# Performance work log

Hardware: AMD Instinct MI355X
Metric: run time of the kernel (lower is better)

Reference implementation:

```python
import jax, jax.numpy as jnp
import numpy as np

LEVELS = 6
_S = float(1.0 / np.sqrt(2.0))  # forward transform scales kernels by 1/sqrt(2)
# Complex Daubechies 6-tap filters (real, imag), pre-scaled for the forward DWT.
LO_R = [v * _S for v in (-0.0662912607, 0.1104854346, 0.6629126074, 0.6629126074, 0.1104854346, -0.0662912607)]
LO_I = [v * _S for v in (-0.0855816496, -0.0855816496, 0.1711632992, 0.1711632992, -0.0855816496, -0.0855816496)]
HI_R = [v * _S for v in (-0.0662912607, -0.1104854346, 0.6629126074, -0.6629126074, 0.1104854346, 0.0662912607)]
HI_I = [v * _S for v in (0.0855816496, -0.0855816496, -0.1711632992, 0.1711632992, 0.0855816496, -0.0855816496)]


def _corr_down(v, k):
    """Circular-padded 6-tap correlation along last axis, stride-2 decimation.
    v: [..., L] (L even) -> [..., L//2]. Matches torch: circular pad 3 each side,
    valid conv (L+1 outputs), then slice 0:-1:2."""
    L = v.shape[-1]
    vp = jnp.concatenate([v[..., -3:], v, v[..., :3]], axis=-1)  # [..., L+6]
    out = k[0] * vp[..., 0:L - 1:2]
    for t in range(1, 6):
        out = out + k[t] * vp[..., t:t + L - 1:2]
    return out


def _cconv_down(xr, xi, kr, ki):
    """Complex conv + downsample: (xr + i*xi) * (kr + i*ki) along last axis."""
    return (_corr_down(xr, kr) - _corr_down(xi, ki),
            _corr_down(xr, ki) + _corr_down(xi, kr))


def _decompose(xr, xi):
    """One DWT level. xr, xi: [B, C, h, w] -> (zr, zi) same shape."""
    # vertical pass: convolve along h (transpose so h is last)
    xrT = xr.swapaxes(-1, -2)  # [B, C, w, h]
    xiT = xi.swapaxes(-1, -2)
    lr, li = _cconv_down(xrT, xiT, LO_R, LO_I)  # [B, C, w, h//2]
    hr, hi = _cconv_down(xrT, xiT, HI_R, HI_I)
    yr = jnp.concatenate([lr, hr], axis=-1).swapaxes(-1, -2)  # [B, C, h, w]
    yi = jnp.concatenate([li, hi], axis=-1).swapaxes(-1, -2)
    # horizontal pass: convolve along w
    lr, li = _cconv_down(yr, yi, LO_R, LO_I)  # [B, C, h, w//2]
    hr, hi = _cconv_down(yr, yi, HI_R, HI_I)
    zr = jnp.concatenate([lr, hr], axis=-1)
    zi = jnp.concatenate([li, hi], axis=-1)
    return zr, zi


def setup_inputs() -> dict:
    key = jax.random.key(0)
    images = jax.random.uniform(key, (8, 3, 1024, 1024), dtype=jnp.float32)
    return {"images": images}


def reference(images):
    B, C, H, W = images.shape
    xr = images
    xi = jnp.zeros_like(images)
    res_r = jnp.zeros((B, C, H, W), images.dtype)
    res_i = jnp.zeros((B, C, H, W), images.dtype)
    for i in range(LEVELS):
        h, w = H >> i, W >> i
        if i == 0:
            sr, si = xr, xi
        else:
            sr, si = res_r[..., :h, :w], res_i[..., :h, :w]
        dr, di = _decompose(sr, si)
        res_r = res_r.at[..., :h, :w].set(dr)
        res_i = res_i.at[..., :h, :w].set(di)
    return jnp.stack([res_r, res_i], axis=2)  # [B, C, 2, H, W]
```

## Files before the change

### kernel.cpp

```cpp
#include <hip/hip_runtime.h>


#define SQ2 0.7071067811865476

constexpr float kLOR0 = (float)(-0.0662912607 * SQ2);
constexpr float kLOR1 = (float)( 0.1104854346 * SQ2);
constexpr float kLOR2 = (float)( 0.6629126074 * SQ2);
constexpr float kLOI0 = (float)(-0.0855816496 * SQ2);
constexpr float kLOI1 = (float)(-0.0855816496 * SQ2);
constexpr float kLOI2 = (float)( 0.1711632992 * SQ2);
constexpr float kHIR0 = (float)(-0.0662912607 * SQ2);
constexpr float kHIR1 = (float)(-0.1104854346 * SQ2);
constexpr float kHIR2 = (float)( 0.6629126074 * SQ2);
constexpr float kHII0 = (float)( 0.0855816496 * SQ2);
constexpr float kHII1 = (float)(-0.0855816496 * SQ2);
constexpr float kHII2 = (float)(-0.1711632992 * SQ2);

typedef float f4v __attribute__((ext_vector_type(4)));

__device__ __forceinline__ void band6(const float* xr, const float* xi,
                                      float& plr, float& pli, float& phr,
                                      float& phi) {
  const float s0 = xr[0] + xr[5], s1 = xr[1] + xr[4], s2 = xr[2] + xr[3];
  const float d0 = xr[0] - xr[5], d1 = xr[1] - xr[4], d2 = xr[2] - xr[3];
  const float t0 = xi[0] + xi[5], t1 = xi[1] + xi[4], t2 = xi[2] + xi[3];
  const float e0 = xi[0] - xi[5], e1 = xi[1] - xi[4], e2 = xi[2] - xi[3];
  plr = (kLOR0 * s0 + kLOR1 * s1 + kLOR2 * s2) -
        (kLOI0 * t0 + kLOI1 * t1 + kLOI2 * t2);
  pli = (kLOI0 * s0 + kLOI1 * s1 + kLOI2 * s2) +
        (kLOR0 * t0 + kLOR1 * t1 + kLOR2 * t2);
  phr = (kHIR0 * d0 + kHIR1 * d1 + kHIR2 * d2) -
        (kHII0 * e0 + kHII1 * e1 + kHII2 * e2);
  phi = (kHII0 * d0 + kHII1 * d1 + kHII2 * d2) +
        (kHIR0 * e0 + kHIR1 * e1 + kHIR2 * e2);
}

__device__ __forceinline__ void gload16(const f4v* src, f4v* ldsDst) {
  __builtin_amdgcn_global_load_lds(
      (__attribute__((address_space(1))) const void*)src,
      (__attribute__((address_space(3))) void*)ldsDst, 16, 0, 0);
}

template <int TB, bool HAS_IMAG, bool LL_TO_WS>
__global__ __launch_bounds__(256) void dwt_kernel(
    const float* __restrict__ inR, const float* __restrict__ inI,
    float* __restrict__ out, float* __restrict__ llR, float* __restrict__ llI,
    int h, int w, int tilesPerRow, int tilesPerPlane, int cpx8, int HW,
    int W0) {
  constexpr int RROWS = 2 * TB + 4;
  constexpr int F4PR = TB / 2 + 2;
  constexpr int SW = 4 * F4PR;
  constexpr int NF4 = RROWS * F4PR;
  constexpr int NF4P = ((NF4 + 255) / 256) * 256;
  constexpr int YW = 2 * TB + 8;
  constexpr int C2 = 2 * TB + 4;
  constexpr int HB = TB / 2;
  constexpr int NJQ4 = TB / 4;

  __shared__ f4v s4R[NF4P];
  __shared__ f4v s4I[HAS_IMAG ? NF4P : 1];
  __shared__ __align__(16) float yLR[HB * YW], yLI[HB * YW];
  __shared__ __align__(16) float yHR[HB * YW], yHI[HB * YW];

  const int tid = threadIdx.x;
  int bid = (int)blockIdx.x;
  bid = (bid & 7) * cpx8 + (bid >> 3);
  const int plane = bid / tilesPerPlane;
  const int trem = bid - plane * tilesPerPlane;
  const int ti = trem / tilesPerRow;
  const int tj = trem - ti * tilesPerRow;

  const int hm = h - 1;
  const int w4 = w >> 2, w4m = w4 - 1;
  const int rowstart = 2 * TB * ti - 3;
  const int col4start = HB * tj - 1;

  const float* pinR = inR + (size_t)plane * h * w;
  const float* pinI = HAS_IMAG ? (inI + (size_t)plane * h * w) : nullptr;

  {
    const int lane = tid & 63;
    const int wid = tid >> 6;
    for (int c0 = wid * 64; c0 < NF4P; c0 += 256) {
      const int idx = c0 + lane;
      const int r = idx / F4PR;
      const int q = idx - r * F4PR;
      const int gr = (rowstart + r) & hm;
      const int gq = (col4start + q) & w4m;
      const size_t goff = (size_t)gr * w4 + gq;
      gload16((const f4v*)pinR + goff, &s4R[c0]);
      if (HAS_IMAG) gload16((const f4v*)pinI + goff, &s4I[c0]);
    }
  }
  __syncthreads();

  const float* sRf = (const float*)s4R;
  const float* sIf = (const float*)s4I;
  const int i0 = TB * ti, j0g = TB * tj;
  const int h2 = h >> 1, w2 = w >> 1;
  float* outR = out + (size_t)plane * 2 * HW;
  float* outI = outR + HW;

#pragma unroll
  for (int p = 0; p < 2; ++p) {
    for (int idx = tid; idx < HB * C2; idx += 256) {
      const int il = idx / C2;
      const int c = idx - il * C2;
      const int rb = 2 * (p * HB + il);
      const float* col = sRf + rb * SW + c + 1;
      const float x0 = col[0], x1 = col[SW], x2 = col[2 * SW];
      const float x3 = col[3 * SW], x4 = col[4 * SW], x5 = col[5 * SW];
      const float sr0 = x0 + x5, sr1 = x1 + x4, sr2 = x2 + x3;
      const float dr0 = x0 - x5, dr1 = x1 - x4, dr2 = x2 - x3;
      float lr = kLOR0 * sr0 + kLOR1 * sr1 + kLOR2 * sr2;
      float li = kLOI0 * sr0 + kLOI1 * sr1 + kLOI2 * sr2;
      float hr = kHIR0 * dr0 + kHIR1 * dr1 + kHIR2 * dr2;
      float hi = kHII0 * dr0 + kHII1 * dr1 + kHII2 * dr2;
      if (HAS_IMAG) {
        const float* colI = sIf + rb * SW + c + 1;
        const float z0 = colI[0], z1 = colI[SW], z2 = colI[2 * SW];
        const float z3 = colI[3 * SW], z4 = colI[4 * SW], z5 = colI[5 * SW];
        const float si0 = z0 + z5, si1 = z1 + z4, si2 = z2 + z3;
        const float di0 = z0 - z5, di1 = z1 - z4, di2 = z2 - z3;
        lr -= kLOI0 * si0 + kLOI1 * si1 + kLOI2 * si2;
        li += kLOR0 * si0 + kLOR1 * si1 + kLOR2 * si2;
        hr -= kHII0 * di0 + kHII1 * di1 + kHII2 * di2;
        hi += kHIR0 * di0 + kHIR1 * di1 + kHIR2 * di2;
      }
      const int yi = il * YW + c;
      yLR[yi] = lr;
      yLI[yi] = li;
      yHR[yi] = hr;
      yHI[yi] = hi;
    }
    __syncthreads();

    const int jq = tid & (NJQ4 - 1);
    const int il = tid / NJQ4;
    if (il < HB) {
      const int base = il * YW + 8 * jq;
      float xLR[12], xLI[12], xHR[12], xHI[12];
      *(f4v*)&xLR[0] = *(const f4v*)&yLR[base];
      *(f4v*)&xLR[4] = *(const f4v*)&yLR[base + 4];
      *(f4v*)&xLR[8] = *(const f4v*)&yLR[base + 8];
      *(f4v*)&xLI[0] = *(const f4v*)&yLI[base];
      *(f4v*)&xLI[4] = *(const f4v*)&yLI[base + 4];
      *(f4v*)&xLI[8] = *(const f4v*)&yLI[base + 8];
      *(f4v*)&xHR[0] = *(const f4v*)&yHR[base];
      *(f4v*)&xHR[4] = *(const f4v*)&yHR[base + 4];
      *(f4v*)&xHR[8] = *(const f4v*)&yHR[base + 8];
      *(f4v*)&xHI[0] = *(const f4v*)&yHI[base];
      *(f4v*)&xHI[4] = *(const f4v*)&yHI[base + 4];
      *(f4v*)&xHI[8] = *(const f4v*)&yHI[base + 8];
      float o[8][4];
#pragma unroll
      for (int u = 0; u < 4; ++u) {
        band6(&xLR[2 * u], &xLI[2 * u], o[0][u], o[1][u], o[2][u], o[3][u]);
        band6(&xHR[2 * u], &xHI[2 * u], o[4][u], o[5][u], o[6][u], o[7][u]);
      }
      const int gi = i0 + p * HB + il;
      const int gj = j0g + 4 * jq;
      const int rlo = gi, rhi = h2 + gi, clo = gj, chi = w2 + gj;
      auto st = [&](float* pdst, int v) {
        f4v t;
        t.x = o[v][0];
        t.y = o[v][1];
        t.z = o[v][2];
        t.w = o[v][3];
        __builtin_nontemporal_store(t, (f4v*)pdst);
      };
      st(outR + (size_t)rlo * W0 + chi, 2);
      st(outI + (size_t)rlo * W0 + chi, 3);
      st(outR + (size_t)rhi * W0 + clo, 4);
      st(outI + (size_t)rhi * W0 + clo, 5);
      st(outR + (size_t)rhi * W0 + chi, 6);
      st(outI + (size_t)rhi * W0 + chi, 7);
      if (LL_TO_WS) {
        const size_t off = (size_t)plane * h2 * w2 + (size_t)gi * w2 + gj;
        f4v a, b;
        a.x = o[0][0];
        a.y = o[0][1];
        a.z = o[0][2];
        a.w = o[0][3];
        b.x = o[1][0];
        b.y = o[1][1];
        b.z = o[1][2];
        b.w = o[1][3];
        *(f4v*)(llR + off) = a;
        *(f4v*)(llI + off) = b;
      } else {
        st(outR + (size_t)rlo * W0 + clo, 0);
        st(outI + (size_t)rlo * W0 + clo, 1);
      }
    }
    __syncthreads();
  }
}

extern "C" void kernel_launch(void* const* d_in, const int* in_sizes, int n_in,
                              void* d_out, int out_size, void* d_ws,
                              size_t ws_size, hipStream_t stream) {
  const float* images = (const float*)d_in[0];
  float* out = (float*)d_out;
  constexpr int B = 8, C = 3, H = 1024, W = 1024;
  constexpr int NP = B * C;

  float* wsf = (float*)d_ws;
  const size_t S0 = (size_t)NP * 512 * 512;
  const size_t S1 = (size_t)NP * 256 * 256;
  float* buf0R = wsf;
  float* buf0I = wsf + S0;
  float* buf1R = wsf + 2 * S0;
  float* buf1I = wsf + 2 * S0 + S1;

  auto launch = [&](auto tb_tag, bool hasImag, bool llToWs, const float* iR,
                    const float* iI, float* lR, float* lI, int hsz) {
    constexpr int TB = decltype(tb_tag)::value;
    const int tpr = (hsz / 2) / TB;
    const int tpp = tpr * tpr;
    const int grid = NP * tpp;
    if (!hasImag) {
      dwt_kernel<TB, false, true><<<grid, 256, 0, stream>>>(
          iR, nullptr, out, lR, lI, hsz, hsz, tpr, tpp, grid / 8, H * W, W);
    } else if (llToWs) {
      dwt_kernel<TB, true, true><<<grid, 256, 0, stream>>>(
          iR, iI, out, lR, lI, hsz, hsz, tpr, tpp, grid / 8, H * W, W);
    } else {
      dwt_kernel<TB, true, false><<<grid, 256, 0, stream>>>(
          iR, iI, out, nullptr, nullptr, hsz, hsz, tpr, tpp, grid / 8, H * W,
          W);
    }
  };

  launch(std::integral_constant<int, 32>{}, false, true, images, nullptr,
         buf0R, buf0I, 1024);
  launch(std::integral_constant<int, 32>{}, true, true, buf0R, buf0I, buf1R,
         buf1I, 512);
  launch(std::integral_constant<int, 32>{}, true, true, buf1R, buf1I, buf0R,
         buf0I, 256);
  launch(std::integral_constant<int, 32>{}, true, true, buf0R, buf0I, buf1R,
         buf1I, 128);
  launch(std::integral_constant<int, 16>{}, true, true, buf1R, buf1I, buf0R,
         buf0I, 64);
  launch(std::integral_constant<int, 16>{}, true, false, buf0R, buf0I,
         nullptr, nullptr, 32);
}
```

Baseline: 98.38 us.

## Split input tile load into halves and overlap second load with horizontal pass

```diff
diff --git a/kernel.cpp b/kernel.cpp
--- a/kernel.cpp
+++ b/kernel.cpp
@@ -1,4 +1,5 @@
 #include <hip/hip_runtime.h>
+#include <type_traits>
 
 
 #define SQ2 0.7071067811865476
@@ -17,22 +18,26 @@
 constexpr float kHII2 = (float)(-0.1711632992 * SQ2);
 
 typedef float f4v __attribute__((ext_vector_type(4)));
-
-__device__ __forceinline__ void band6(const float* xr, const float* xi,
-                                      float& plr, float& pli, float& phr,
-                                      float& phi) {
+typedef float f2v __attribute__((ext_vector_type(2)));
+
+template <bool IM>
+__device__ __forceinline__ void cconv6(const float* xr, const float* xi,
+                                       float& lr, float& li, float& hr,
+                                       float& hi) {
   const float s0 = xr[0] + xr[5], s1 = xr[1] + xr[4], s2 = xr[2] + xr[3];
   const float d0 = xr[0] - xr[5], d1 = xr[1] - xr[4], d2 = xr[2] - xr[3];
-  const float t0 = xi[0] + xi[5], t1 = xi[1] + xi[4], t2 = xi[2] + xi[3];
-  const float e0 = xi[0] - xi[5], e1 = xi[1] - xi[4], e2 = xi[2] - xi[3];
-  plr = (kLOR0 * s0 + kLOR1 * s1 + kLOR2 * s2) -
-        (kLOI0 * t0 + kLOI1 * t1 + kLOI2 * t2);
-  pli = (kLOI0 * s0 + kLOI1 * s1 + kLOI2 * s2) +
-        (kLOR0 * t0 + kLOR1 * t1 + kLOR2 * t2);
-  phr = (kHIR0 * d0 + kHIR1 * d1 + kHIR2 * d2) -
-        (kHII0 * e0 + kHII1 * e1 + kHII2 * e2);
-  phi = (kHII0 * d0 + kHII1 * d1 + kHII2 * d2) +
-        (kHIR0 * e0 + kHIR1 * e1 + kHIR2 * e2);
+  lr = kLOR0 * s0 + kLOR1 * s1 + kLOR2 * s2;
+  li = kLOI0 * s0 + kLOI1 * s1 + kLOI2 * s2;
+  hr = kHIR0 * d0 + kHIR1 * d1 + kHIR2 * d2;
+  hi = kHII0 * d0 + kHII1 * d1 + kHII2 * d2;
+  if (IM) {
+    const float t0 = xi[0] + xi[5], t1 = xi[1] + xi[4], t2 = xi[2] + xi[3];
+    const float e0 = xi[0] - xi[5], e1 = xi[1] - xi[4], e2 = xi[2] - xi[3];
+    lr -= kLOI0 * t0 + kLOI1 * t1 + kLOI2 * t2;
+    li += kLOR0 * t0 + kLOR1 * t1 + kLOR2 * t2;
+    hr -= kHII0 * e0 + kHII1 * e1 + kHII2 * e2;
+    hi += kHIR0 * e0 + kHIR1 * e1 + kHIR2 * e2;
+  }
 }
 
 __device__ __forceinline__ void gload16(const f4v* src, f4v* ldsDst) {
@@ -47,18 +52,19 @@
     float* __restrict__ out, float* __restrict__ llR, float* __restrict__ llI,
     int h, int w, int tilesPerRow, int tilesPerPlane, int cpx8, int HW,
     int W0) {
-  constexpr int RROWS = 2 * TB + 4;
+  constexpr int RH = TB + 5;
   constexpr int F4PR = TB / 2 + 2;
   constexpr int SW = 4 * F4PR;
-  constexpr int NF4 = RROWS * F4PR;
-  constexpr int NF4P = ((NF4 + 255) / 256) * 256;
-  constexpr int YW = 2 * TB + 8;
+  constexpr int NF4H = RH * F4PR;
+  constexpr int NF4HP = ((NF4H + 63) / 64) * 64;
   constexpr int C2 = 2 * TB + 4;
+  constexpr int YW = C2;
   constexpr int HB = TB / 2;
   constexpr int NJQ4 = TB / 4;
-
-  __shared__ f4v s4R[NF4P];
-  __shared__ f4v s4I[HAS_IMAG ? NF4P : 1];
+  constexpr int NU = TB + 2;
+
+  __shared__ f4v s4R[NF4HP];
+  __shared__ f4v s4I[HAS_IMAG ? NF4HP : 1];
   __shared__ __align__(16) float yLR[HB * YW], yLI[HB * YW];
   __shared__ __align__(16) float yHR[HB * YW], yHI[HB * YW];
 
@@ -72,16 +78,23 @@
 
   const int hm = h - 1;
   const int w4 = w >> 2, w4m = w4 - 1;
-  const int rowstart = 2 * TB * ti - 3;
   const int col4start = HB * tj - 1;
 
   const float* pinR = inR + (size_t)plane * h * w;
   const float* pinI = HAS_IMAG ? (inI + (size_t)plane * h * w) : nullptr;
 
-  {
+  const float* sRf = (const float*)s4R;
+  const float* sIf = (const float*)s4I;
+  const int i0 = TB * ti, j0g = TB * tj;
+  const int h2 = h >> 1, w2 = w >> 1;
+  float* outR = out + (size_t)plane * 2 * HW;
+  float* outI = outR + HW;
+
+  auto stage1 = [&](int p) {
+    const int rowstart = 2 * TB * ti + TB * p - 3;
     const int lane = tid & 63;
     const int wid = tid >> 6;
-    for (int c0 = wid * 64; c0 < NF4P; c0 += 256) {
+    for (int c0 = wid * 64; c0 < NF4HP; c0 += 256) {
       const int idx = c0 + lane;
       const int r = idx / F4PR;
       const int q = idx - r * F4PR;
@@ -91,50 +104,68 @@
       gload16((const f4v*)pinR + goff, &s4R[c0]);
       if (HAS_IMAG) gload16((const f4v*)pinI + goff, &s4I[c0]);
     }
-  }
-  __syncthreads();
-
-  const float* sRf = (const float*)s4R;
-  const float* sIf = (const float*)s4I;
-  const int i0 = TB * ti, j0g = TB * tj;
-  const int h2 = h >> 1, w2 = w >> 1;
-  float* outR = out + (size_t)plane * 2 * HW;
-  float* outI = outR + HW;
-
-#pragma unroll
-  for (int p = 0; p < 2; ++p) {
-    for (int idx = tid; idx < HB * C2; idx += 256) {
-      const int il = idx / C2;
-      const int c = idx - il * C2;
-      const int rb = 2 * (p * HB + il);
-      const float* col = sRf + rb * SW + c + 1;
-      const float x0 = col[0], x1 = col[SW], x2 = col[2 * SW];
-      const float x3 = col[3 * SW], x4 = col[4 * SW], x5 = col[5 * SW];
-      const float sr0 = x0 + x5, sr1 = x1 + x4, sr2 = x2 + x3;
-      const float dr0 = x0 - x5, dr1 = x1 - x4, dr2 = x2 - x3;
-      float lr = kLOR0 * sr0 + kLOR1 * sr1 + kLOR2 * sr2;
-      float li = kLOI0 * sr0 + kLOI1 * sr1 + kLOI2 * sr2;
-      float hr = kHIR0 * dr0 + kHIR1 * dr1 + kHIR2 * dr2;
-      float hi = kHII0 * dr0 + kHII1 * dr1 + kHII2 * dr2;
-      if (HAS_IMAG) {
-        const float* colI = sIf + rb * SW + c + 1;
-        const float z0 = colI[0], z1 = colI[SW], z2 = colI[2 * SW];
-        const float z3 = colI[3 * SW], z4 = colI[4 * SW], z5 = colI[5 * SW];
-        const float si0 = z0 + z5, si1 = z1 + z4, si2 = z2 + z3;
-        const float di0 = z0 - z5, di1 = z1 - z4, di2 = z2 - z3;
-        lr -= kLOI0 * si0 + kLOI1 * si1 + kLOI2 * si2;
-        li += kLOR0 * si0 + kLOR1 * si1 + kLOR2 * si2;
-        hr -= kHII0 * di0 + kHII1 * di1 + kHII2 * di2;
-        hi += kHIR0 * di0 + kHIR1 * di1 + kHIR2 * di2;
+  };
+
+  auto stage2 = [&]() {
+    for (int idx = tid; idx < HB * NU; idx += 256) {
+      const int il = idx / NU;
+      const int u = idx - il * NU;
+      const int yo = il * YW;
+      const float* bR = sRf + 2 * il * SW;
+      const float* bI = sIf + 2 * il * SW;
+      if (u == 0) {
+        float ar[6], ai[6];
+        float lr, li, hr, hi;
+#pragma unroll
+        for (int k = 0; k < 6; ++k) {
+          ar[k] = bR[k * SW + 1];
+          if (HAS_IMAG) ai[k] = bI[k * SW + 1];
+        }
+        cconv6<HAS_IMAG>(ar, ai, lr, li, hr, hi);
+        yLR[yo] = lr;
+        yLI[yo] = li;
+        yHR[yo] = hr;
+        yHI[yo] = hi;
+#pragma unroll
+        for (int k = 0; k < 6; ++k) {
+          ar[k] = bR[k * SW + C2];
+          if (HAS_IMAG) ai[k] = bI[k * SW + C2];
+        }
+        cconv6<HAS_IMAG>(ar, ai, lr, li, hr, hi);
+        yLR[yo + C2 - 1] = lr;
+        yLI[yo + C2 - 1] = li;
+        yHR[yo + C2 - 1] = hr;
+        yHI[yo + C2 - 1] = hi;
+      } else {
+        const int cc = 2 * u;
+        float ar[6], ai[6], br[6], bi[6];
+#pragma unroll
+        for (int k = 0; k < 6; ++k) {
+          const f2v v = *(const f2v*)(bR + k * SW + cc);
+          ar[k] = v.x;
+          br[k] = v.y;
+          if (HAS_IMAG) {
+            const f2v z = *(const f2v*)(bI + k * SW + cc);
+            ai[k] = z.x;
+            bi[k] = z.y;
+          }
+        }
+        float lr0, li0, hr0, hi0, lr1, li1, hr1, hi1;
+        cconv6<HAS_IMAG>(ar, ai, lr0, li0, hr0, hi0);
+        cconv6<HAS_IMAG>(br, bi, lr1, li1, hr1, hi1);
+        yLR[yo + cc - 1] = lr0;
+        yLR[yo + cc] = lr1;
+        yLI[yo + cc - 1] = li0;
+        yLI[yo + cc] = li1;
+        yHR[yo + cc - 1] = hr0;
+        yHR[yo + cc] = hr1;
+        yHI[yo + cc - 1] = hi0;
+        yHI[yo + cc] = hi1;
       }
-      const int yi = il * YW + c;
-      yLR[yi] = lr;
-      yLI[yi] = li;
-      yHR[yi] = hr;
-      yHI[yi] = hi;
-    }
-    __syncthreads();
-
+    }
+  };
+
+  auto stage3 = [&](int p) {
     const int jq = tid & (NJQ4 - 1);
     const int il = tid / NJQ4;
     if (il < HB) {
@@ -155,8 +186,10 @@
       float o[8][4];
 #pragma unroll
       for (int u = 0; u < 4; ++u) {
-        band6(&xLR[2 * u], &xLI[2 * u], o[0][u], o[1][u], o[2][u], o[3][u]);
-        band6(&xHR[2 * u], &xHI[2 * u], o[4][u], o[5][u], o[6][u], o[7][u]);
+        cconv6<true>(&xLR[2 * u], &xLI[2 * u], o[0][u], o[1][u], o[2][u],
+                     o[3][u]);
+        cconv6<true>(&xHR[2 * u], &xHI[2 * u], o[4][u], o[5][u], o[6][u],
+                     o[7][u]);
       }
       const int gi = i0 + p * HB + il;
       const int gj = j0g + 4 * jq;
@@ -193,8 +226,18 @@
         st(outI + (size_t)rlo * W0 + clo, 1);
       }
     }
-    __syncthreads();
-  }
+  };
+
+  stage1(0);
+  __syncthreads();
+  stage2();
+  __syncthreads();
+  stage1(1);
+  stage3(0);
+  __syncthreads();
+  stage2();
+  __syncthreads();
+  stage3(1);
 }
 
 extern "C" void kernel_launch(void* const* d_in, const int* in_sizes, int n_in,
```

New measurement: 104.6 us. 6.3% more time.

## Make DWT stages wave-private to drop block-wide barriers between passes

Applied to the files above, without the earlier changes.

```diff
diff --git a/kernel.cpp b/kernel.cpp
--- a/kernel.cpp
+++ b/kernel.cpp
@@ -1,4 +1,5 @@
 #include <hip/hip_runtime.h>
+#include <type_traits>
 
 
 #define SQ2 0.7071067811865476
@@ -17,22 +18,26 @@
 constexpr float kHII2 = (float)(-0.1711632992 * SQ2);
 
 typedef float f4v __attribute__((ext_vector_type(4)));
-
-__device__ __forceinline__ void band6(const float* xr, const float* xi,
-                                      float& plr, float& pli, float& phr,
-                                      float& phi) {
+typedef float f2v __attribute__((ext_vector_type(2)));
+
+template <bool IM>
+__device__ __forceinline__ void cconv6(const float* xr, const float* xi,
+                                       float& lr, float& li, float& hr,
+                                       float& hi) {
   const float s0 = xr[0] + xr[5], s1 = xr[1] + xr[4], s2 = xr[2] + xr[3];
   const float d0 = xr[0] - xr[5], d1 = xr[1] - xr[4], d2 = xr[2] - xr[3];
-  const float t0 = xi[0] + xi[5], t1 = xi[1] + xi[4], t2 = xi[2] + xi[3];
-  const float e0 = xi[0] - xi[5], e1 = xi[1] - xi[4], e2 = xi[2] - xi[3];
-  plr = (kLOR0 * s0 + kLOR1 * s1 + kLOR2 * s2) -
-        (kLOI0 * t0 + kLOI1 * t1 + kLOI2 * t2);
-  pli = (kLOI0 * s0 + kLOI1 * s1 + kLOI2 * s2) +
-        (kLOR0 * t0 + kLOR1 * t1 + kLOR2 * t2);
-  phr = (kHIR0 * d0 + kHIR1 * d1 + kHIR2 * d2) -
-        (kHII0 * e0 + kHII1 * e1 + kHII2 * e2);
-  phi = (kHII0 * d0 + kHII1 * d1 + kHII2 * d2) +
-        (kHIR0 * e0 + kHIR1 * e1 + kHIR2 * e2);
+  lr = kLOR0 * s0 + kLOR1 * s1 + kLOR2 * s2;
+  li = kLOI0 * s0 + kLOI1 * s1 + kLOI2 * s2;
+  hr = kHIR0 * d0 + kHIR1 * d1 + kHIR2 * d2;
+  hi = kHII0 * d0 + kHII1 * d1 + kHII2 * d2;
+  if (IM) {
+    const float t0 = xi[0] + xi[5], t1 = xi[1] + xi[4], t2 = xi[2] + xi[3];
+    const float e0 = xi[0] - xi[5], e1 = xi[1] - xi[4], e2 = xi[2] - xi[3];
+    lr -= kLOI0 * t0 + kLOI1 * t1 + kLOI2 * t2;
+    li += kLOR0 * t0 + kLOR1 * t1 + kLOR2 * t2;
+    hr -= kHII0 * e0 + kHII1 * e1 + kHII2 * e2;
+    hi += kHIR0 * e0 + kHIR1 * e1 + kHIR2 * e2;
+  }
 }
 
 __device__ __forceinline__ void gload16(const f4v* src, f4v* ldsDst) {
@@ -52,15 +57,14 @@
   constexpr int SW = 4 * F4PR;
   constexpr int NF4 = RROWS * F4PR;
   constexpr int NF4P = ((NF4 + 255) / 256) * 256;
-  constexpr int YW = 2 * TB + 8;
   constexpr int C2 = 2 * TB + 4;
-  constexpr int HB = TB / 2;
-  constexpr int NJQ4 = TB / 4;
+  constexpr int NPASS = TB / 16;
+  constexpr int QACT = (TB / 2 < 16) ? TB / 2 : 16;
 
   __shared__ f4v s4R[NF4P];
   __shared__ f4v s4I[HAS_IMAG ? NF4P : 1];
-  __shared__ __align__(16) float yLR[HB * YW], yLI[HB * YW];
-  __shared__ __align__(16) float yHR[HB * YW], yHI[HB * YW];
+  __shared__ __align__(16) float yLR[16 * C2], yLI[16 * C2];
+  __shared__ __align__(16) float yHR[16 * C2], yHI[16 * C2];
 
   const int tid = threadIdx.x;
   int bid = (int)blockIdx.x;
@@ -73,7 +77,7 @@
   const int hm = h - 1;
   const int w4 = w >> 2, w4m = w4 - 1;
   const int rowstart = 2 * TB * ti - 3;
-  const int col4start = HB * tj - 1;
+  const int col4start = (TB / 2) * tj - 1;
 
   const float* pinR = inR + (size_t)plane * h * w;
   const float* pinI = HAS_IMAG ? (inI + (size_t)plane * h * w) : nullptr;
@@ -83,10 +87,10 @@
     const int wid = tid >> 6;
     for (int c0 = wid * 64; c0 < NF4P; c0 += 256) {
       const int idx = c0 + lane;
-      const int r = idx / F4PR;
-      const int q = idx - r * F4PR;
-      const int gr = (rowstart + r) & hm;
-      const int gq = (col4start + q) & w4m;
+      const int rr = idx / F4PR;
+      const int qq = idx - rr * F4PR;
+      const int gr = (rowstart + rr) & hm;
+      const int gq = (col4start + qq) & w4m;
       const size_t goff = (size_t)gr * w4 + gq;
       gload16((const f4v*)pinR + goff, &s4R[c0]);
       if (HAS_IMAG) gload16((const f4v*)pinI + goff, &s4I[c0]);
@@ -101,73 +105,90 @@
   float* outR = out + (size_t)plane * 2 * HW;
   float* outI = outR + HW;
 
-#pragma unroll
-  for (int p = 0; p < 2; ++p) {
-    for (int idx = tid; idx < HB * C2; idx += 256) {
-      const int il = idx / C2;
-      const int c = idx - il * C2;
-      const int rb = 2 * (p * HB + il);
-      const float* col = sRf + rb * SW + c + 1;
-      const float x0 = col[0], x1 = col[SW], x2 = col[2 * SW];
-      const float x3 = col[3 * SW], x4 = col[4 * SW], x5 = col[5 * SW];
-      const float sr0 = x0 + x5, sr1 = x1 + x4, sr2 = x2 + x3;
-      const float dr0 = x0 - x5, dr1 = x1 - x4, dr2 = x2 - x3;
-      float lr = kLOR0 * sr0 + kLOR1 * sr1 + kLOR2 * sr2;
-      float li = kLOI0 * sr0 + kLOI1 * sr1 + kLOI2 * sr2;
-      float hr = kHIR0 * dr0 + kHIR1 * dr1 + kHIR2 * dr2;
-      float hi = kHII0 * dr0 + kHII1 * dr1 + kHII2 * dr2;
-      if (HAS_IMAG) {
-        const float* colI = sIf + rb * SW + c + 1;
-        const float z0 = colI[0], z1 = colI[SW], z2 = colI[2 * SW];
-        const float z3 = colI[3 * SW], z4 = colI[4 * SW], z5 = colI[5 * SW];
-        const float si0 = z0 + z5, si1 = z1 + z4, si2 = z2 + z3;
-        const float di0 = z0 - z5, di1 = z1 - z4, di2 = z2 - z3;
-        lr -= kLOI0 * si0 + kLOI1 * si1 + kLOI2 * si2;
-        li += kLOR0 * si0 + kLOR1 * si1 + kLOR2 * si2;
-        hr -= kHII0 * di0 + kHII1 * di1 + kHII2 * di2;
-        hi += kHIR0 * di0 + kHIR1 * di1 + kHIR2 * di2;
+  const int wv = tid >> 6;
+  const int lane = tid & 63;
+  const int r = lane >> 4, q = lane & 15;
+
+  for (int p = 0; p < NPASS; ++p) {
+    const int ibase = p * 16 + wv * 4;
+
+    {
+      auto s2col = [&](int c) {
+        const float* cR = sRf + (2 * ibase) * SW + c + 1;
+        const float* cI = sIf + (2 * ibase) * SW + c + 1;
+        float xr[12], xi[12];
+#pragma unroll
+        for (int m = 0; m < 12; ++m) {
+          xr[m] = cR[m * SW];
+          if (HAS_IMAG) xi[m] = cI[m * SW];
+        }
+#pragma unroll
+        for (int k = 0; k < 4; ++k) {
+          float lr, li, hr, hi;
+          cconv6<HAS_IMAG>(&xr[2 * k], &xi[2 * k], lr, li, hr, hi);
+          const int yi = (wv * 4 + k) * C2 + c;
+          yLR[yi] = lr;
+          yLI[yi] = li;
+          yHR[yi] = hr;
+          yHI[yi] = hi;
+        }
+      };
+      if (C2 >= 64) {
+        s2col(lane);
+        if (lane < 4 * (C2 - 64)) {
+          const int ce = 64 + (lane >> 2);
+          const int ke = lane & 3;
+          const float* cR = sRf + (2 * (ibase + ke)) * SW + ce + 1;
+          const float* cI = sIf + (2 * (ibase + ke)) * SW + ce + 1;
+          float xr[6], xi[6];
+#pragma unroll
+          for (int m = 0; m < 6; ++m) {
+            xr[m] = cR[m * SW];
+            if (HAS_IMAG) xi[m] = cI[m * SW];
+          }
+          float lr, li, hr, hi;
+          cconv6<HAS_IMAG>(xr, xi, lr, li, hr, hi);
+          const int yi = (wv * 4 + ke) * C2 + ce;
+          yLR[yi] = lr;
+          yLI[yi] = li;
+          yHR[yi] = hr;
+          yHI[yi] = hi;
+        }
+      } else {
+        if (lane < C2) s2col(lane);
       }
-      const int yi = il * YW + c;
-      yLR[yi] = lr;
-      yLI[yi] = li;
-      yHR[yi] = hr;
-      yHI[yi] = hi;
-    }
-    __syncthreads();
-
-    const int jq = tid & (NJQ4 - 1);
-    const int il = tid / NJQ4;
-    if (il < HB) {
-      const int base = il * YW + 8 * jq;
-      float xLR[12], xLI[12], xHR[12], xHI[12];
+    }
+    asm volatile("s_waitcnt lgkmcnt(0)" ::: "memory");
+    __builtin_amdgcn_sched_barrier(0);
+
+    if (q < QACT) {
+      const int slot = wv * 4 + r;
+      const int base = slot * C2 + 4 * q;
+      float xLR[8], xLI[8], xHR[8], xHI[8];
       *(f4v*)&xLR[0] = *(const f4v*)&yLR[base];
       *(f4v*)&xLR[4] = *(const f4v*)&yLR[base + 4];
-      *(f4v*)&xLR[8] = *(const f4v*)&yLR[base + 8];
       *(f4v*)&xLI[0] = *(const f4v*)&yLI[base];
       *(f4v*)&xLI[4] = *(const f4v*)&yLI[base + 4];
-      *(f4v*)&xLI[8] = *(const f4v*)&yLI[base + 8];
       *(f4v*)&xHR[0] = *(const f4v*)&yHR[base];
       *(f4v*)&xHR[4] = *(const f4v*)&yHR[base + 4];
-      *(f4v*)&xHR[8] = *(const f4v*)&yHR[base + 8];
       *(f4v*)&xHI[0] = *(const f4v*)&yHI[base];
       *(f4v*)&xHI[4] = *(const f4v*)&yHI[base + 4];
-      *(f4v*)&xHI[8] = *(const f4v*)&yHI[base + 8];
-      float o[8][4];
-#pragma unroll
-      for (int u = 0; u < 4; ++u) {
-        band6(&xLR[2 * u], &xLI[2 * u], o[0][u], o[1][u], o[2][u], o[3][u]);
-        band6(&xHR[2 * u], &xHI[2 * u], o[4][u], o[5][u], o[6][u], o[7][u]);
+      float o[8][2];
+#pragma unroll
+      for (int u = 0; u < 2; ++u) {
+        cconv6<true>(&xLR[2 * u], &xLI[2 * u], o[0][u], o[1][u], o[2][u],
+                     o[3][u]);
+        cconv6<true>(&xHR[2 * u], &xHI[2 * u], o[4][u], o[5][u], o[6][u],
+                     o[7][u]);
       }
-      const int gi = i0 + p * HB + il;
-      const int gj = j0g + 4 * jq;
+      const int gi = i0 + ibase + r;
+      const int gj = j0g + 2 * q;
       const int rlo = gi, rhi = h2 + gi, clo = gj, chi = w2 + gj;
       auto st = [&](float* pdst, int v) {
-        f4v t;
+        f2v t;
         t.x = o[v][0];
         t.y = o[v][1];
-        t.z = o[v][2];
-        t.w = o[v][3];
-        __builtin_nontemporal_store(t, (f4v*)pdst);
+        __builtin_nontemporal_store(t, (f2v*)pdst);
       };
       st(outR + (size_t)rlo * W0 + chi, 2);
       st(outI + (size_t)rlo * W0 + chi, 3);
@@ -177,23 +198,18 @@
       st(outI + (size_t)rhi * W0 + chi, 7);
       if (LL_TO_WS) {
         const size_t off = (size_t)plane * h2 * w2 + (size_t)gi * w2 + gj;
-        f4v a, b;
+        f2v a, b;
         a.x = o[0][0];
         a.y = o[0][1];
-        a.z = o[0][2];
-        a.w = o[0][3];
         b.x = o[1][0];
         b.y = o[1][1];
-        b.z = o[1][2];
-        b.w = o[1][3];
-        *(f4v*)(llR + off) = a;
-        *(f4v*)(llI + off) = b;
+        *(f2v*)(llR + off) = a;
+        *(f2v*)(llI + off) = b;
       } else {
         st(outR + (size_t)rlo * W0 + clo, 0);
         st(outI + (size_t)rlo * W0 + clo, 1);
       }
     }
-    __syncthreads();
   }
 }
 
```

Result: faster. 89.02 us, median of 2 (-9.5%).
